# Performance work log

Hardware: AMD Instinct MI355X
Metric: run time of the kernel (lower is better)

The kernel has to match this reference:

```python
import jax, jax.numpy as jnp
import numpy as np

DIM = 1024
HEADS = 16
HEAD_DIM = DIM // HEADS
FF_MULT = 2
ROPE_BASE = 10000.0
EPS = 1e-6
B, S = 2, 2048


def setup_inputs() -> dict:
    key = jax.random.key(0)
    ks = jax.random.split(key, 6)
    sc = lambda fan_in: 1.0 / np.sqrt(fan_in)
    return {
        "x": jax.random.normal(ks[0], (B, S, DIM), dtype=jnp.float32),
        "w_in_norm": jnp.ones((DIM,), dtype=jnp.float32),
        "w_ff_norm": jnp.ones((DIM,), dtype=jnp.float32),
        "w_qkv": jax.random.normal(ks[1], (3 * DIM, DIM), dtype=jnp.float32) * sc(DIM),
        "w_out": jax.random.normal(ks[2], (DIM, DIM), dtype=jnp.float32) * sc(DIM),
        "w_fc": jax.random.normal(ks[3], (DIM * FF_MULT, DIM), dtype=jnp.float32) * sc(DIM),
        "w_proj": jax.random.normal(ks[4], (DIM, DIM * FF_MULT), dtype=jnp.float32) * sc(DIM * FF_MULT),
    }


def rmsnorm(x, w):
    var = jnp.mean(jnp.square(x), axis=-1, keepdims=True)
    return x * jax.lax.rsqrt(var + EPS) * w


def rope_tables(seq_len):
    half = HEAD_DIM // 2
    inv_freq = 1.0 / (ROPE_BASE ** (2.0 * jnp.arange(half, dtype=jnp.float32) / HEAD_DIM))
    angles = jnp.arange(seq_len, dtype=jnp.float32)[:, None] * inv_freq[None, :]  # (S, half)
    return jnp.cos(angles), jnp.sin(angles)


def apply_rope(x, cos, sin):
    # x: (B, H, S, D); interleaved pairs along last dim
    xp = x.reshape(*x.shape[:-1], HEAD_DIM // 2, 2)
    x_even, x_odd = xp[..., 0], xp[..., 1]
    c = cos.astype(x.dtype)  # (S, half) broadcasts over (B, H)
    s = sin.astype(x.dtype)
    rot_even = x_even * c - x_odd * s
    rot_odd = x_odd * c + x_even * s
    return jnp.stack([rot_even, rot_odd], axis=-1).reshape(x.shape)


def reference(x, w_in_norm, w_ff_norm, w_qkv, w_out, w_fc, w_proj):
    b, s, d = x.shape
    # --- attention sub-block (pre-norm) ---
    h = rmsnorm(x, w_in_norm)
    qkv = jnp.einsum("bsd,ed->bse", h, w_qkv)  # (B, S, 3*D)
    q, k, v = jnp.split(qkv, 3, axis=-1)
    def heads(t):
        return t.reshape(b, s, HEADS, HEAD_DIM).transpose(0, 2, 1, 3)  # (B, H, S, Dh)
    q, k, v = heads(q), heads(k), heads(v)
    cos, sin = rope_tables(s)
    q = apply_rope(q, cos, sin)
    k = apply_rope(k, cos, sin)
    scale = 1.0 / np.sqrt(HEAD_DIM)
    scores = jnp.einsum("bhqd,bhkd->bhqk", q, k) * scale
    causal = jnp.tril(jnp.ones((s, s), dtype=bool))
    scores = jnp.where(causal, scores, jnp.finfo(scores.dtype).min)
    probs = jax.nn.softmax(scores, axis=-1)
    attn = jnp.einsum("bhqk,bhkd->bhqd", probs, v)
    attn = attn.transpose(0, 2, 1, 3).reshape(b, s, d)
    x = x + jnp.einsum("bsd,ed->bse", attn, w_out)
    # --- feed-forward sub-block (pre-norm) ---
    h = rmsnorm(x, w_ff_norm)
    hid = jax.nn.silu(jnp.einsum("bsd,fd->bsf", h, w_fc))
    x = x + jnp.einsum("bsf,df->bsd", hid, w_proj)
    return x
```

## Files before the change

kernel.cpp:

```cpp
#include <hip/hip_runtime.h>
#include <hip/hip_bf16.h>
#include <cstdint>

#define DIMSZ 1024
#define S_LEN 2048
#define NH 16
#define HD 64

typedef __attribute__((ext_vector_type(4))) float f32x4;
typedef __attribute__((ext_vector_type(8))) __bf16 bf16x8;

#define MFMA_BF16(a,b,c) __builtin_amdgcn_mfma_f32_16x16x32_bf16((a),(b),(c),0,0,0)

__device__ __forceinline__ void gload_lds16(const void* g, void* l) {
  __builtin_amdgcn_global_load_lds(
      (const __attribute__((address_space(1))) unsigned int*)(uintptr_t)g,
      (__attribute__((address_space(3))) unsigned int*)(uintptr_t)l,
      16, 0, 0);
}

__global__ __launch_bounds__(256)
void cast_all_kernel(const float* __restrict__ s0, const float* __restrict__ s1,
                     const float* __restrict__ s2, const float* __restrict__ s3,
                     __hip_bfloat16* __restrict__ d0, __hip_bfloat16* __restrict__ d1,
                     __hip_bfloat16* __restrict__ d2, __hip_bfloat16* __restrict__ d3)
{
  int i = blockIdx.x * 256 + threadIdx.x;
  const float* s; __hip_bfloat16* d; int off;
  if (i < 786432)       { s = s0; d = d0; off = i; }
  else if (i < 1048576) { s = s1; d = d1; off = i - 786432; }
  else if (i < 1572864) { s = s2; d = d2; off = i - 1048576; }
  else                  { s = s3; d = d3; off = i - 1572864; }
  float4 v = ((const float4*)s)[off];
  __hip_bfloat16* o = d + (size_t)off * 4;
  o[0] = __float2bfloat16(v.x);
  o[1] = __float2bfloat16(v.y);
  o[2] = __float2bfloat16(v.z);
  o[3] = __float2bfloat16(v.w);
}

__global__ __launch_bounds__(256)
void rmsnorm_kernel(const float* __restrict__ x, const float* __restrict__ w,
                    __hip_bfloat16* __restrict__ out)
{
  int row = blockIdx.x;
  int tid = threadIdx.x;
  const float4 v = ((const float4*)(x + (size_t)row * DIMSZ))[tid];
  float ss = v.x*v.x + v.y*v.y + v.z*v.z + v.w*v.w;
  #pragma unroll
  for (int m = 32; m >= 1; m >>= 1) ss += __shfl_xor(ss, m);
  __shared__ float red[4];
  int wave = tid >> 6, lane = tid & 63;
  if (lane == 0) red[wave] = ss;
  __syncthreads();
  float tot = red[0] + red[1] + red[2] + red[3];
  float sc = rsqrtf(tot * (1.0f / DIMSZ) + 1e-6f);
  const float4 wv = ((const float4*)w)[tid];
  __hip_bfloat16* o = out + (size_t)row * DIMSZ + tid * 4;
  o[0] = __float2bfloat16(v.x * sc * wv.x);
  o[1] = __float2bfloat16(v.y * sc * wv.y);
  o[2] = __float2bfloat16(v.z * sc * wv.z);
  o[3] = __float2bfloat16(v.w * sc * wv.w);
}

template<int EPI>
__global__ __launch_bounds__(256, 2)
void gemm_bt2(const __hip_bfloat16* __restrict__ A,
              const __hip_bfloat16* __restrict__ Bw,
              float* __restrict__ Cf,
              __hip_bfloat16* __restrict__ Cb,
              const float* __restrict__ resid,
              int N, int K)
{
  __shared__ __align__(16) char sA[2][16384];
  __shared__ __align__(16) char sB[2][16384];
  const int tid = threadIdx.x;
  const int wave = tid >> 6, lane = tid & 63;
  const int lg = lane >> 4, lr15 = lane & 15;
  const int row0 = blockIdx.y * 128, col0 = blockIdx.x * 128;
  const int wr = wave >> 1, wc = wave & 1;
  f32x4 acc[4][4] = {};

  const size_t Kb = (size_t)K * 2;
  const int rown = tid >> 3;
  const int scol = ((tid & 7) << 4) ^ ((rown & 7) << 4);
  const char* gA = (const char*)A + (size_t)(row0 + rown) * Kb + scol;
  const char* gB = (const char*)Bw + (size_t)(col0 + rown) * Kb + scol;
  const int dbase = wave * 1024;

  const int nsteps = K >> 6;
  int cur = 0;

#define STAGE_G(buf, st) do {                                              \
    const size_t kb_ = (size_t)(st) * 128;                                 \
    _Pragma("unroll")                                                      \
    for (int it = 0; it < 4; ++it) {                                       \
      gload_lds16(gA + (size_t)(it * 32) * Kb + kb_, &sA[buf][it * 4096 + dbase]); \
      gload_lds16(gB + (size_t)(it * 32) * Kb + kb_, &sB[buf][it * 4096 + dbase]); \
    }                                                                      \
  } while (0)

  STAGE_G(0, 0);
  __syncthreads();

  const int swz = (lr15 & 7) << 4;
  for (int st = 0; st < nsteps; ++st) {
    if (st + 1 < nsteps) STAGE_G(cur ^ 1, st + 1);
    const char* pA = sA[cur];
    const char* pB = sB[cur];
    bf16x8 af[2][4], bfr[2][4];
    #pragma unroll
    for (int m = 0; m < 4; ++m) {
      const int ra = (wr * 64 + m * 16 + lr15) * 128;
      af[0][m] = *(const bf16x8*)(pA + ra + ((lg * 16) ^ swz));
      af[1][m] = *(const bf16x8*)(pA + ra + ((64 + lg * 16) ^ swz));
      const int rb = (wc * 64 + m * 16 + lr15) * 128;
      bfr[0][m] = *(const bf16x8*)(pB + rb + ((lg * 16) ^ swz));
      bfr[1][m] = *(const bf16x8*)(pB + rb + ((64 + lg * 16) ^ swz));
    }
    #pragma unroll
    for (int kh = 0; kh < 2; ++kh)
      #pragma unroll
      for (int m = 0; m < 4; ++m)
        #pragma unroll
        for (int n = 0; n < 4; ++n)
          acc[m][n] = MFMA_BF16(af[kh][m], bfr[kh][n], acc[m][n]);
    __syncthreads();
    cur ^= 1;
  }
#undef STAGE_G

  #pragma unroll
  for (int m = 0; m < 4; ++m) {
    #pragma unroll
    for (int n = 0; n < 4; ++n) {
      #pragma unroll
      for (int r = 0; r < 4; ++r) {
        const int grow = row0 + wr * 64 + m * 16 + lg * 4 + r;
        const int gcol = col0 + wc * 64 + n * 16 + lr15;
        const size_t idx = (size_t)grow * N + gcol;
        const float v = acc[m][n][r];
        if (EPI == 0) {
          Cb[idx] = __float2bfloat16(v);
        } else if (EPI == 1) {
          Cf[idx] = resid[idx] + v;
        } else {
          Cb[idx] = __float2bfloat16(v / (1.0f + __expf(-v)));
        }
      }
    }
  }
}

__global__ __launch_bounds__(256)
void rope_qk(const __hip_bfloat16* __restrict__ qkv,
             __hip_bfloat16* __restrict__ Q, __hip_bfloat16* __restrict__ Kx)
{
  int idx = blockIdx.x * 256 + threadIdx.x;
  int i = idx & 31;
  int h = (idx >> 5) & 15;
  int s = (idx >> 9) & (S_LEN - 1);
  int b = idx >> 20;
  const size_t base = ((size_t)b * S_LEN + s) * 3072 + h * 64 + 2 * i;
  float qe = __bfloat162float(qkv[base]);
  float qo = __bfloat162float(qkv[base + 1]);
  float ke = __bfloat162float(qkv[base + 1024]);
  float ko = __bfloat162float(qkv[base + 1025]);
  float inv = __expf(-(2.0f * i) * (9.210340371976184f / 64.0f));
  float ang = (float)s * inv;
  float sn, cs;
  __sincosf(ang, &sn, &cs);
  const float sc = 0.125f;
  size_t qb = (((size_t)b * NH + h) * S_LEN + s) * HD + 2 * i;
  Q[qb]     = __float2bfloat16((qe * cs - qo * sn) * sc);
  Q[qb + 1] = __float2bfloat16((qo * cs + qe * sn) * sc);
  Kx[qb]     = __float2bfloat16(ke * cs - ko * sn);
  Kx[qb + 1] = __float2bfloat16(ko * cs + ke * sn);
}

__global__ __launch_bounds__(256)
void v_transpose(const __hip_bfloat16* __restrict__ qkv, __hip_bfloat16* __restrict__ Vt)
{
  __shared__ __hip_bfloat16 t[64][72];
  const int s0 = blockIdx.x * 64;
  const int bh = blockIdx.y;
  const int b = bh >> 4, h = bh & 15;
  const int tid = threadIdx.x;
  const int c = tid & 63;
  #pragma unroll
  for (int r = 0; r < 16; ++r) {
    int srow = r * 4 + (tid >> 6);
    t[srow][c] = qkv[((size_t)b * S_LEN + s0 + srow) * 3072 + 2048 + h * 64 + c];
  }
  __syncthreads();
  #pragma unroll
  for (int r = 0; r < 16; ++r) {
    int drow = r * 4 + (tid >> 6);
    Vt[(((size_t)b * NH + h) * HD + drow) * S_LEN + s0 + c] = t[c][drow];
  }
}

__device__ __forceinline__ unsigned bf16pack2(float a, float b) {
  __hip_bfloat16 ha = __float2bfloat16(a), hb = __float2bfloat16(b);
  unsigned ua = *reinterpret_cast<unsigned short*>(&ha);
  unsigned ub = *reinterpret_cast<unsigned short*>(&hb);
  return ua | (ub << 16);
}

__global__ __launch_bounds__(256, 4)
void flash_attn3(const __hip_bfloat16* __restrict__ Q,
                 const __hip_bfloat16* __restrict__ Kx,
                 const __hip_bfloat16* __restrict__ Vt,
                 __hip_bfloat16* __restrict__ attn)
{
  __shared__ __align__(16) char sK[2][8192];
  __shared__ __align__(16) char sV[2][8192];
  __shared__ __align__(16) char sP[4][2048];

  const int tid = threadIdx.x;
  const int w = tid >> 6;
  const int lane = tid & 63;
  const int lg = lane >> 4, lr = lane & 15;
  const int bid = blockIdx.x;
  const int bh = bid & 31;
  const int b = bh >> 4, h = bh & 15;
  const int j = bid >> 5;
  const int m = j >> 3, a = j & 7;
  const int xm = (0x6170 >> (m << 2)) & 7;
  const int qb = m * 8 + (a ^ xm);
  const int q0 = qb * 64;
  const int nsteps = qb + 1;

  const char* Kb = (const char*)(Kx + (size_t)bh * S_LEN * HD);
  const char* Vb = (const char*)(Vt + (size_t)bh * HD * S_LEN);
  const __hip_bfloat16* Qp = Q + (size_t)bh * S_LEN * HD;

  const int q0w = q0 + w * 16;
  const bf16x8 qf0 = *(const bf16x8*)&Qp[(q0w + lr) * HD + lg * 8];
  const bf16x8 qf1 = *(const bf16x8*)&Qp[(q0w + lr) * HD + 32 + lg * 8];
  char* sPw = sP[w];
  const int swzr = (lr & 7) << 4;
  const int wbase = (tid & 192) << 4;

  f32x4 acc[4] = {};
  float lsum = 0.f;
  int cur = 0;

  #pragma unroll
  for (int i = 0; i < 2; ++i) {
    const int c = i * 256 + tid;
    const int row = c >> 3;
    const int scol = ((c & 7) << 4) ^ ((row & 7) << 4);
    gload_lds16(Kb + (size_t)row * 128 + scol, sK[0] + i * 4096 + wbase);
    gload_lds16(Vb + (size_t)row * (S_LEN * 2) + scol, sV[0] + i * 4096 + wbase);
  }
  __syncthreads();

  for (int st = 0; st < nsteps; ++st) {
    if (st + 1 < nsteps) {
      const int kn = (st + 1) * 64;
      #pragma unroll
      for (int i = 0; i < 2; ++i) {
        const int c = i * 256 + tid;
        const int row = c >> 3;
        const int scol = ((c & 7) << 4) ^ ((row & 7) << 4);
        gload_lds16(Kb + (size_t)(kn + row) * 128 + scol, sK[cur ^ 1] + i * 4096 + wbase);
        gload_lds16(Vb + (size_t)row * (S_LEN * 2) + (size_t)kn * 2 + scol, sV[cur ^ 1] + i * 4096 + wbase);
      }
    }
    const int k0 = st * 64;
    const char* pK = sK[cur];
    const char* pV = sV[cur];
    f32x4 sv[4];
    #pragma unroll
    for (int t = 0; t < 4; ++t) {
      const int rb = (t * 16 + lr) * 128;
      const bf16x8 kf0 = *(const bf16x8*)(pK + rb + ((lg * 16) ^ swzr));
      const bf16x8 kf1 = *(const bf16x8*)(pK + rb + ((64 + lg * 16) ^ swzr));
      f32x4 z = {};
      z = MFMA_BF16(kf0, qf0, z);
      z = MFMA_BF16(kf1, qf1, z);
      sv[t] = z;
    }
    const bool maskstep = (st == nsteps - 1);
    #pragma unroll
    for (int t = 0; t < 4; ++t) {
      float p[4];
      #pragma unroll
      for (int r = 0; r < 4; ++r) {
        float e = __expf(fminf(sv[t][r], 30.f));
        if (maskstep) {
          const int kg = k0 + t * 16 + lg * 4 + r;
          e = (kg <= q0w + lr) ? e : 0.f;
        }
        lsum += e;
        p[r] = e;
      }
      uint2 wv2;
      wv2.x = bf16pack2(p[0], p[1]);
      wv2.y = bf16pack2(p[2], p[3]);
      *(uint2*)(sPw + lr * 128 + ((t * 32 + lg * 8) ^ swzr)) = wv2;
    }
    asm volatile("s_waitcnt lgkmcnt(0)" ::: "memory");
    __builtin_amdgcn_sched_barrier(0);
    const bf16x8 pa0 = *(const bf16x8*)(sPw + lr * 128 + ((lg * 16) ^ swzr));
    const bf16x8 pa1 = *(const bf16x8*)(sPw + lr * 128 + ((64 + lg * 16) ^ swzr));
    #pragma unroll
    for (int dt = 0; dt < 4; ++dt) {
      const int rb = (dt * 16 + lr) * 128;
      const bf16x8 vf0 = *(const bf16x8*)(pV + rb + ((lg * 16) ^ swzr));
      const bf16x8 vf1 = *(const bf16x8*)(pV + rb + ((64 + lg * 16) ^ swzr));
      acc[dt] = MFMA_BF16(pa0, vf0, acc[dt]);
      acc[dt] = MFMA_BF16(pa1, vf1, acc[dt]);
    }
    __syncthreads();
    cur ^= 1;
  }

  lsum += __shfl_xor(lsum, 16);
  lsum += __shfl_xor(lsum, 32);
  #pragma unroll
  for (int r = 0; r < 4; ++r) {
    const float li = __shfl(lsum, lg * 4 + r);
    const float rli = 1.0f / li;
    const size_t rowb = ((size_t)b * S_LEN + q0w + lg * 4 + r) * DIMSZ + h * HD;
    #pragma unroll
    for (int dt = 0; dt < 4; ++dt)
      attn[rowb + dt * 16 + lr] = __float2bfloat16(acc[dt][r] * rli);
  }
}

extern "C" void kernel_launch(void* const* d_in, const int* in_sizes, int n_in,
                              void* d_out, int out_size, void* d_ws, size_t ws_size,
                              hipStream_t stream)
{
  const float* x      = (const float*)d_in[0];
  const float* w_in   = (const float*)d_in[1];
  const float* w_ff   = (const float*)d_in[2];
  const float* w_qkv  = (const float*)d_in[3];
  const float* w_out  = (const float*)d_in[4];
  const float* w_fc   = (const float*)d_in[5];
  const float* w_proj = (const float*)d_in[6];
  float* out = (float*)d_out;
  char* ws = (char*)d_ws;

  __hip_bfloat16* wq_b   = (__hip_bfloat16*)(ws);
  __hip_bfloat16* wo_b   = (__hip_bfloat16*)(ws + 6291456);
  __hip_bfloat16* wfc_b  = (__hip_bfloat16*)(ws + 8388608);
  __hip_bfloat16* wpr_b  = (__hip_bfloat16*)(ws + 12582912);
  __hip_bfloat16* h_b    = (__hip_bfloat16*)(ws + 16777216);
  __hip_bfloat16* qkv_b  = (__hip_bfloat16*)(ws + 25165824);
  __hip_bfloat16* attn_b = (__hip_bfloat16*)(ws + 25165824);
  __hip_bfloat16* hid_b  = (__hip_bfloat16*)(ws + 33554432);
  __hip_bfloat16* Q_b    = (__hip_bfloat16*)(ws + 50331648);
  __hip_bfloat16* K_b    = (__hip_bfloat16*)(ws + 58720256);
  __hip_bfloat16* Vt_b   = (__hip_bfloat16*)(ws + 67108864);
  float*          x1     = (float*)(ws + 50331648);

  cast_all_kernel<<<8192, 256, 0, stream>>>(w_qkv, w_out, w_fc, w_proj, wq_b, wo_b, wfc_b, wpr_b);
  rmsnorm_kernel<<<4096, 256, 0, stream>>>(x, w_in, h_b);
  gemm_bt2<0><<<dim3(3072 / 128, 4096 / 128), 256, 0, stream>>>(h_b, wq_b, nullptr, qkv_b, nullptr, 3072, 1024);
  rope_qk<<<2097152 / 256, 256, 0, stream>>>(qkv_b, Q_b, K_b);
  v_transpose<<<dim3(32, 32), 256, 0, stream>>>(qkv_b, Vt_b);
  flash_attn3<<<1024, 256, 0, stream>>>(Q_b, K_b, Vt_b, attn_b);
  gemm_bt2<1><<<dim3(1024 / 128, 4096 / 128), 256, 0, stream>>>(attn_b, wo_b, x1, nullptr, x, 1024, 1024);
  rmsnorm_kernel<<<4096, 256, 0, stream>>>(x1, w_ff, h_b);
  gemm_bt2<2><<<dim3(2048 / 128, 4096 / 128), 256, 0, stream>>>(h_b, wfc_b, nullptr, hid_b, nullptr, 2048, 1024);
  gemm_bt2<1><<<dim3(1024 / 128, 4096 / 128), 256, 0, stream>>>(hid_b, wpr_b, out, nullptr, x1, 1024, 2048);
}
```

Measured before the change: 174.8 us.

## Add 256x256 ping-pong GEMM for QKV and FC, raise MFMA priority in attention

Adds a new 512-thread GEMM kernel with 256x256 tiles, double-buffered LDS staging interleaved with MFMA phases, XCD-aware block swizzling and s_setprio around MFMA bursts. It is used for the QKV and FC projections in place of the 128x128 kernel, to raise data reuse per loaded tile and overlap loads with compute. The attention kernel also gets setprio hints around its MFMA loops and drops the fminf clamp before exp. The large tiles give only 192 and 128 blocks, which may underfill the GPU. Removing the clamp risks overflow if scores grow large.

```diff
diff --git a/kernel.cpp b/kernel.cpp
--- a/kernel.cpp
+++ b/kernel.cpp
@@ -61,6 +61,124 @@
   o[1] = __float2bfloat16(v.y * sc * wv.y);
   o[2] = __float2bfloat16(v.z * sc * wv.z);
   o[3] = __float2bfloat16(v.w * sc * wv.w);
+}
+
+template<int EPI>
+__global__ __launch_bounds__(512, 2)
+void gemm256(const __hip_bfloat16* __restrict__ A,
+             const __hip_bfloat16* __restrict__ Bw,
+             float* __restrict__ Cf, __hip_bfloat16* __restrict__ Cb,
+             const float* __restrict__ resid,
+             int N, int K, int nbx)
+{
+  __shared__ __align__(16) char sA[2][32768];
+  __shared__ __align__(16) char sB[2][32768];
+  const int tid = threadIdx.x;
+  const int w = tid >> 6, lane = tid & 63;
+  const int lg = lane >> 4, lr = lane & 15;
+  const int wr = w >> 2, wc = w & 3;
+  const int cpx = gridDim.x >> 3;
+  const int swb = (blockIdx.x & 7) * cpx + (blockIdx.x >> 3);
+  const int bx = swb % nbx, by = swb / nbx;
+  const int row0 = by * 256, col0 = bx * 256;
+
+  const size_t Kb = (size_t)K * 2;
+  const int rr = tid >> 3;
+  const int scol = ((tid & 7) << 4) ^ ((rr & 7) << 4);
+  const char* gA = (const char*)A + (size_t)(row0 + rr) * Kb + scol;
+  const char* gB = (const char*)Bw + (size_t)(col0 + rr) * Kb + scol;
+  const int wofs = w << 10;
+
+  f32x4 acc[8][4] = {};
+
+#define SA_(buf, kt, hf) do { \
+    gload_lds16(gA + (size_t)((hf) * 128) * Kb + (size_t)(kt) * 128, sA[buf] + (hf) * 16384 + wofs); \
+    gload_lds16(gA + (size_t)((hf) * 128 + 64) * Kb + (size_t)(kt) * 128, sA[buf] + (hf) * 16384 + 8192 + wofs); \
+  } while (0)
+#define SB_(buf, kt, hf) do { \
+    gload_lds16(gB + (size_t)((hf) * 128) * Kb + (size_t)(kt) * 128, sB[buf] + (hf) * 16384 + wofs); \
+    gload_lds16(gB + (size_t)((hf) * 128 + 64) * Kb + (size_t)(kt) * 128, sB[buf] + (hf) * 16384 + 8192 + wofs); \
+  } while (0)
+
+  SB_(0, 0, 0); SB_(0, 0, 1); SA_(0, 0, 0); SA_(0, 0, 1);
+  SB_(1, 1, 0); SB_(1, 1, 1); SA_(1, 1, 0);
+  __syncthreads();
+
+  const int swz = (lr & 7) << 4;
+  const int ntiles = K >> 6;
+  const int niter = ntiles >> 1;
+  const int abase = wr * 16384;
+  const int bbase = (wc >> 1) * 16384 + ((wc & 1) * 64) * 128;
+  const int c0 = (lg * 16) ^ swz;
+  const int c1 = (64 + lg * 16) ^ swz;
+
+  bf16x8 br_[4][2];
+
+#define LOADB(par) do { _Pragma("unroll") for (int n = 0; n < 4; ++n) { \
+    const char* p = sB[par] + bbase + (n * 16 + lr) * 128; \
+    br_[n][0] = *(const bf16x8*)(p + c0); br_[n][1] = *(const bf16x8*)(p + c1); } } while (0)
+
+#define PHASE(par, q, STAGE_STMT) do { \
+    bf16x8 a0k0, a0k1, a1k0, a1k1; \
+    { const char* p = sA[par] + abase + ((q) * 32 + lr) * 128; \
+      a0k0 = *(const bf16x8*)(p + c0); a0k1 = *(const bf16x8*)(p + c1); } \
+    { const char* p = sA[par] + abase + ((q) * 32 + 16 + lr) * 128; \
+      a1k0 = *(const bf16x8*)(p + c0); a1k1 = *(const bf16x8*)(p + c1); } \
+    STAGE_STMT; \
+    __builtin_amdgcn_s_barrier(); \
+    asm volatile("s_waitcnt lgkmcnt(0)" ::: "memory"); \
+    __builtin_amdgcn_sched_barrier(0); \
+    __builtin_amdgcn_s_setprio(1); \
+    _Pragma("unroll") for (int n = 0; n < 4; ++n) { \
+      acc[(q)*2][n]   = MFMA_BF16(a0k0, br_[n][0], acc[(q)*2][n]); \
+      acc[(q)*2+1][n] = MFMA_BF16(a1k0, br_[n][0], acc[(q)*2+1][n]); } \
+    _Pragma("unroll") for (int n = 0; n < 4; ++n) { \
+      acc[(q)*2][n]   = MFMA_BF16(a0k1, br_[n][1], acc[(q)*2][n]); \
+      acc[(q)*2+1][n] = MFMA_BF16(a1k1, br_[n][1], acc[(q)*2+1][n]); } \
+    __builtin_amdgcn_s_setprio(0); \
+    __builtin_amdgcn_s_barrier(); \
+  } while (0)
+
+  for (int it = 0; it < niter; ++it) {
+    const int T0 = 2 * it, T1 = T0 + 1;
+    LOADB(0);
+    PHASE(0, 0, { SA_(1, T1, 1); });
+    PHASE(0, 1, { if (T0 + 2 < ntiles) SB_(0, T0 + 2, 0); });
+    PHASE(0, 2, { if (T0 + 2 < ntiles) SB_(0, T0 + 2, 1); });
+    PHASE(0, 3, { if (T0 + 2 < ntiles) SA_(0, T0 + 2, 0);
+                  asm volatile("s_waitcnt vmcnt(6)" ::: "memory"); });
+    LOADB(1);
+    PHASE(1, 0, { if (T0 + 2 < ntiles) SA_(0, T0 + 2, 1); });
+    PHASE(1, 1, { if (T1 + 2 < ntiles) SB_(1, T1 + 2, 0); });
+    PHASE(1, 2, { if (T1 + 2 < ntiles) SB_(1, T1 + 2, 1); });
+    PHASE(1, 3, { if (T1 + 2 < ntiles) SA_(1, T1 + 2, 0);
+                  asm volatile("s_waitcnt vmcnt(6)" ::: "memory"); });
+  }
+#undef SA_
+#undef SB_
+#undef LOADB
+#undef PHASE
+
+  #pragma unroll
+  for (int m = 0; m < 8; ++m) {
+    #pragma unroll
+    for (int n = 0; n < 4; ++n) {
+      #pragma unroll
+      for (int r = 0; r < 4; ++r) {
+        const int grow = row0 + wr * 128 + m * 16 + lg * 4 + r;
+        const int gcol = col0 + wc * 64 + n * 16 + lr;
+        const size_t idx = (size_t)grow * N + gcol;
+        const float v = acc[m][n][r];
+        if (EPI == 0) {
+          Cb[idx] = __float2bfloat16(v);
+        } else if (EPI == 1) {
+          Cf[idx] = resid[idx] + v;
+        } else {
+          Cb[idx] = __float2bfloat16(v / (1.0f + __expf(-v)));
+        }
+      }
+    }
+  }
 }
 
 template<int EPI>
@@ -272,6 +390,7 @@
     const char* pK = sK[cur];
     const char* pV = sV[cur];
     f32x4 sv[4];
+    __builtin_amdgcn_s_setprio(1);
     #pragma unroll
     for (int t = 0; t < 4; ++t) {
       const int rb = (t * 16 + lr) * 128;
@@ -282,13 +401,14 @@
       z = MFMA_BF16(kf1, qf1, z);
       sv[t] = z;
     }
+    __builtin_amdgcn_s_setprio(0);
     const bool maskstep = (st == nsteps - 1);
     #pragma unroll
     for (int t = 0; t < 4; ++t) {
       float p[4];
       #pragma unroll
       for (int r = 0; r < 4; ++r) {
-        float e = __expf(fminf(sv[t][r], 30.f));
+        float e = __expf(sv[t][r]);
         if (maskstep) {
           const int kg = k0 + t * 16 + lg * 4 + r;
           e = (kg <= q0w + lr) ? e : 0.f;
@@ -305,6 +425,7 @@
     __builtin_amdgcn_sched_barrier(0);
     const bf16x8 pa0 = *(const bf16x8*)(sPw + lr * 128 + ((lg * 16) ^ swzr));
     const bf16x8 pa1 = *(const bf16x8*)(sPw + lr * 128 + ((64 + lg * 16) ^ swzr));
+    __builtin_amdgcn_s_setprio(1);
     #pragma unroll
     for (int dt = 0; dt < 4; ++dt) {
       const int rb = (dt * 16 + lr) * 128;
@@ -313,6 +434,7 @@
       acc[dt] = MFMA_BF16(pa0, vf0, acc[dt]);
       acc[dt] = MFMA_BF16(pa1, vf1, acc[dt]);
     }
+    __builtin_amdgcn_s_setprio(0);
     __syncthreads();
     cur ^= 1;
   }
@@ -359,12 +481,12 @@
 
   cast_all_kernel<<<8192, 256, 0, stream>>>(w_qkv, w_out, w_fc, w_proj, wq_b, wo_b, wfc_b, wpr_b);
   rmsnorm_kernel<<<4096, 256, 0, stream>>>(x, w_in, h_b);
-  gemm_bt2<0><<<dim3(3072 / 128, 4096 / 128), 256, 0, stream>>>(h_b, wq_b, nullptr, qkv_b, nullptr, 3072, 1024);
+  gemm256<0><<<dim3(192), 512, 0, stream>>>(h_b, wq_b, nullptr, qkv_b, nullptr, 3072, 1024, 12);
   rope_qk<<<2097152 / 256, 256, 0, stream>>>(qkv_b, Q_b, K_b);
   v_transpose<<<dim3(32, 32), 256, 0, stream>>>(qkv_b, Vt_b);
   flash_attn3<<<1024, 256, 0, stream>>>(Q_b, K_b, Vt_b, attn_b);
   gemm_bt2<1><<<dim3(1024 / 128, 4096 / 128), 256, 0, stream>>>(attn_b, wo_b, x1, nullptr, x, 1024, 1024);
   rmsnorm_kernel<<<4096, 256, 0, stream>>>(x1, w_ff, h_b);
-  gemm_bt2<2><<<dim3(2048 / 128, 4096 / 128), 256, 0, stream>>>(h_b, wfc_b, nullptr, hid_b, nullptr, 2048, 1024);
+  gemm256<2><<<dim3(128), 512, 0, stream>>>(h_b, wfc_b, nullptr, hid_b, nullptr, 2048, 1024, 8);
   gemm_bt2<1><<<dim3(1024 / 128, 4096 / 128), 256, 0, stream>>>(hid_b, wpr_b, out, nullptr, x1, 1024, 2048);
 }
```

Result: slower. 187.9 us (+7.5%).
